# Kernel tuning notes

Hardware: AMD Instinct MI355X
Metric: run time of the kernel (lower is better)

## Reference

```python
import jax, jax.numpy as jnp
import numpy as np

B, S, DIM = 2, 2048, 1024
H, DH = 16, 64  # num_head, head_dim


def setup_inputs() -> dict:
    key = jax.random.key(0)
    ks = jax.random.split(key, 9)
    s = 1.0 / np.sqrt(DIM)
    s2 = 1.0 / np.sqrt(H * DH)
    return {
        "X": jax.random.normal(ks[0], (B, S, DIM), dtype=jnp.float32),
        "mask": jnp.ones((B, S), dtype=jnp.float32),
        "Wq": jax.random.normal(ks[1], (DIM, H * DH), dtype=jnp.float32) * s,
        "bq": jax.random.normal(ks[2], (H * DH,), dtype=jnp.float32) * s,
        "Wk": jax.random.normal(ks[3], (DIM, H * DH), dtype=jnp.float32) * s,
        "bk": jax.random.normal(ks[4], (H * DH,), dtype=jnp.float32) * s,
        "Wv": jax.random.normal(ks[5], (DIM, H * DH), dtype=jnp.float32) * s,
        "bv": jax.random.normal(ks[6], (H * DH,), dtype=jnp.float32) * s,
        "Wo": jax.random.normal(ks[7], (H * DH, DIM), dtype=jnp.float32) * s2,
        "bo": jax.random.normal(ks[8], (DIM,), dtype=jnp.float32) * s2,
    }


def _split_heads(x):
    # [B,S,H*DH] -> [B,H,S,DH]
    return x.reshape(B, S, H, DH).transpose(0, 2, 1, 3)


def reference(X, mask, Wq, bq, Wk, bk, Wv, bv, Wo, bo):
    Q = _split_heads(X @ Wq + bq)
    K = _split_heads(X @ Wk + bk)
    V = _split_heads(X @ Wv + bv)
    # scores: [B,H,S,S]
    dot = jnp.einsum("bhqd,bhkd->bhqk", Q, K) / np.sqrt(DH).astype(np.float32)
    dot = dot - 1000000.0 * (1.0 - mask[:, None, None, :])
    attn = jax.nn.softmax(dot, axis=-1)
    ctx = jnp.einsum("bhqk,bhkd->bhqd", attn, V)
    # combine heads: [B,S,H*DH]
    ctx = ctx.transpose(0, 2, 1, 3).reshape(B, S, H * DH)
    return ctx @ Wo + bo
```

## Files before the change

kernel.cpp:

```cpp
#include <hip/hip_runtime.h>
#include <hip/hip_bf16.h>
#include <math.h>

#define BB 2
#define SS 2048
#define DIM 1024
#define NH 16
#define DH 64

typedef __bf16 bf16x8 __attribute__((ext_vector_type(8)));
typedef float f32x4 __attribute__((ext_vector_type(4)));
typedef float f32x16 __attribute__((ext_vector_type(16)));
typedef unsigned int u32x4 __attribute__((ext_vector_type(4)));

#define PENL2 (1000000.0f * 1.44269504f)

#define VMW(N) asm volatile("s_waitcnt vmcnt(" #N ")" ::: "memory")

__device__ __forceinline__ void glds16(const __hip_bfloat16* g, __hip_bfloat16* l) {
    __builtin_amdgcn_global_load_lds(
        (const __attribute__((address_space(1))) void*)g,
        (__attribute__((address_space(3))) void*)l, 16, 0, 0);
}

__device__ __forceinline__ void glds4(const float* g, float* l) {
    __builtin_amdgcn_global_load_lds(
        (const __attribute__((address_space(1))) void*)g,
        (__attribute__((address_space(3))) void*)l, 4, 0, 0);
}

__device__ __forceinline__ unsigned short f2bf(float x) {
    unsigned int u = __builtin_bit_cast(unsigned int, x);
    return (unsigned short)((u + 0x8000u) >> 16);
}

__device__ __forceinline__ unsigned int pk2bf(float a, float b) {
#if __has_builtin(__builtin_amdgcn_cvt_pk_bf16_f32)
    typedef __bf16 bf16x2 __attribute__((ext_vector_type(2)));
    bf16x2 p = __builtin_amdgcn_cvt_pk_bf16_f32(a, b);
    return __builtin_bit_cast(unsigned int, p);
#else
    return (unsigned int)f2bf(a) | ((unsigned int)f2bf(b) << 16);
#endif
}

__device__ __forceinline__ float fexp2(float x) {
#if __has_builtin(__builtin_amdgcn_exp2f)
    return __builtin_amdgcn_exp2f(x);
#else
    return exp2f(x);
#endif
}

__device__ __forceinline__ float frcp(float x) {
#if __has_builtin(__builtin_amdgcn_rcpf)
    return __builtin_amdgcn_rcpf(x);
#else
    return 1.0f / x;
#endif
}

__global__ void prep(const float* __restrict__ X,
                     const float* __restrict__ Wq, const float* __restrict__ Wk,
                     const float* __restrict__ Wv, const float* __restrict__ Wo,
                     const float* __restrict__ mask, float* __restrict__ pf,
                     __hip_bfloat16* __restrict__ T4, ushort4* __restrict__ Xbf) {
    int z = blockIdx.z;
    int t = threadIdx.x;
    if (z == 4) {
        int c = blockIdx.y * 32 + blockIdx.x;
        const float4* in = (const float4*)X;
#pragma unroll
        for (int k = 0; k < 4; ++k) {
            int i = c * 1024 + k * 256 + t;
            float4 v = in[i];
            ushort4 h;
            h.x = f2bf(v.x); h.y = f2bf(v.y); h.z = f2bf(v.z); h.w = f2bf(v.w);
            Xbf[i] = h;
        }
        if (c < 16) {
            int i = c * 256 + t;
            pf[i] = -PENL2 * (1.0f - mask[i]);
        }
        return;
    }
    const float* W = (z == 0) ? Wq : (z == 1) ? Wk : (z == 2) ? Wv : Wo;
    __hip_bfloat16* Thi = T4 + (size_t)z * DIM * DIM;
    __shared__ float tile[32][33];
    int k0 = blockIdx.x * 32, n0 = blockIdx.y * 32;
    int r = t >> 3, c = (t & 7) << 2;
    float4 v = *(const float4*)&W[(size_t)(k0 + r) * DIM + n0 + c];
    tile[r][c] = v.x; tile[r][c + 1] = v.y; tile[r][c + 2] = v.z; tile[r][c + 3] = v.w;
    __syncthreads();
    size_t base = (size_t)(n0 + r) * DIM + k0 + c;
#pragma unroll
    for (int i = 0; i < 4; ++i)
        ((unsigned short*)Thi)[base + i] = f2bf(tile[c + i][r]);
}

#define BM 128
#define BK 32
#define QSCALE (0.125f * 1.44269504f)
template <int TBN>
__global__ __launch_bounds__(512, 6) void gemm_bf(
    const __hip_bfloat16* __restrict__ A, const __hip_bfloat16* __restrict__ B,
    const float* __restrict__ b0, const float* __restrict__ b1, const float* __restrict__ b2,
    __hip_bfloat16* __restrict__ oq, __hip_bfloat16* __restrict__ ok,
    __hip_bfloat16* __restrict__ ov, float* __restrict__ of32, int mode) {
    __shared__ alignas(16) __hip_bfloat16 sA[3][BM * BK];
    __shared__ alignas(16) __hip_bfloat16 sB[3][TBN * BK];
    const int K = 1024;
    const int JF = TBN / 64;
    int tid = threadIdx.x;
    int wave = tid >> 6, lane = tid & 63, quad = lane >> 4, l16 = lane & 15;

    int nbx = gridDim.x;
    int nwg = nbx * gridDim.y;
    int bid = blockIdx.y * nbx + blockIdx.x;
    int swz = (bid & 7) * (nwg >> 3) + (bid >> 3);
    int m0 = (swz / nbx) * BM, n0 = (swz % nbx) * TBN;
    int mo = (wave >> 2) * 64, no = (wave & 3) * (TBN / 4);

    f32x4 acc[4][JF];
#pragma unroll
    for (int i = 0; i < 4; ++i)
#pragma unroll
        for (int j = 0; j < JF; ++j) acc[i][j] = (f32x4){0.f, 0.f, 0.f, 0.f};

    int ar = tid >> 2;
    int c4 = tid & 3;
    int cs = c4 ^ ((ar >> 1) & 3);
    const __hip_bfloat16* gA = A + (size_t)(m0 + ar) * K + cs * 8;
    const __hip_bfloat16* gB = B + (size_t)(n0 + ar) * K + cs * 8;
    int ldst = ar * BK + c4 * 8;
    bool stgB = (ar < TBN);

    auto STG = [&](int bb, int k0) {
        glds16(gA + k0, &sA[bb][ldst]);
        if (stgB) glds16(gB + k0, &sB[bb][ldst]);
    };

    STG(0, 0);
    STG(1, BK);
    int cur = 0;
    for (int it = 0; it < 32; ++it) {
        int k0 = it * BK;
        if (it < 30) {
            int nb = cur + 2; if (nb >= 3) nb -= 3;
            STG(nb, k0 + 2 * BK);
            if (stgB) { VMW(4); } else { VMW(2); }
        } else if (it == 30) {
            if (stgB) { VMW(2); } else { VMW(1); }
        } else {
            VMW(0);
        }
        __builtin_amdgcn_s_barrier();

        bf16x8 a_h[4], b_h[JF];
#pragma unroll
        for (int i = 0; i < 4; ++i) {
            int rr = mo + i * 16 + l16;
            int ph = quad ^ ((rr >> 1) & 3);
            a_h[i] = *(const bf16x8*)&sA[cur][rr * BK + ph * 8];
        }
#pragma unroll
        for (int j = 0; j < JF; ++j) {
            int rr = no + j * 16 + l16;
            int ph = quad ^ ((rr >> 1) & 3);
            b_h[j] = *(const bf16x8*)&sB[cur][rr * BK + ph * 8];
        }
        __builtin_amdgcn_s_setprio(1);
#pragma unroll
        for (int i = 0; i < 4; ++i)
#pragma unroll
            for (int j = 0; j < JF; ++j)
                acc[i][j] = __builtin_amdgcn_mfma_f32_16x16x32_bf16(a_h[i], b_h[j], acc[i][j], 0, 0, 0);
        __builtin_amdgcn_s_setprio(0);
        __builtin_amdgcn_s_barrier();
        cur = (cur == 2) ? 0 : cur + 1;
    }

    int which = (mode == 1) ? (n0 >> 10) : 0;
    const float* bp = (mode == 0) ? b0 : (which == 0) ? b0 : (which == 1) ? b1 : b2;
#pragma unroll
    for (int i = 0; i < 4; ++i)
#pragma unroll
        for (int j = 0; j < JF; ++j) {
            int gmb = m0 + mo + i * 16 + quad * 4;
            int gn  = n0 + no + j * 16 + l16;
            int nn  = gn & 1023;
            float bb = bp[(mode == 0) ? gn : nn];
#pragma unroll
            for (int r = 0; r < 4; ++r) {
                int gm = gmb + r;
                float v = acc[i][j][r] + bb;
                if (mode == 0) {
                    of32[(size_t)gm * 1024 + gn] = v;
                } else {
                    int b = gm >> 11, s = gm & 2047, h = nn >> 6, d = nn & 63;
                    if (which == 0)
                        ((unsigned short*)oq)[(((size_t)(b * NH + h)) * SS + s) * DH + d] = f2bf(v * QSCALE);
                    else if (which == 1)
                        ((unsigned short*)ok)[(((size_t)(b * NH + h)) * SS + s) * DH + d] = f2bf(v);
                    else
                        ((unsigned short*)ov)[(((size_t)(b * NH + h)) * DH + d) * SS + s] = f2bf(v);
                }
            }
        }
}

__global__ __launch_bounds__(512, 4) void gemm_of(
    const __hip_bfloat16* __restrict__ O1, const __hip_bfloat16* __restrict__ O2,
    const float* __restrict__ l1, const float* __restrict__ l2,
    const __hip_bfloat16* __restrict__ Bw,
    const float* __restrict__ bias, float* __restrict__ out) {
    __shared__ alignas(16) __hip_bfloat16 sA[2][BM * BK];
    __shared__ alignas(16) __hip_bfloat16 sB[2][64 * BK];
    int tid = threadIdx.x;
    int wave = tid >> 6, lane = tid & 63, quad = lane >> 4, l16 = lane & 15;

    int nbx = gridDim.x;
    int nwg = nbx * gridDim.y;
    int bid = blockIdx.y * nbx + blockIdx.x;
    int swz = (bid & 7) * (nwg >> 3) + (bid >> 3);
    int m0 = (swz / nbx) * BM, n0 = (swz % nbx) * 64;
    int mo = (wave >> 2) * 64, no = (wave & 3) * 16;

    f32x4 acc[4];
#pragma unroll
    for (int i = 0; i < 4; ++i) acc[i] = (f32x4){0.f, 0.f, 0.f, 0.f};

    int ar = tid >> 2;
    int c4 = tid & 3;
    int cs = c4 ^ ((ar >> 1) & 3);
    int m  = m0 + ar;
    int bq16 = (m >> 11) * NH;
    int sq   = m & 2047;
    const __hip_bfloat16* gO1 = O1 + (size_t)m * 1024 + cs * 8;
    const __hip_bfloat16* gO2 = O2 + (size_t)m * 1024 + cs * 8;
    const __hip_bfloat16* gB  = Bw + (size_t)(n0 + ar) * 1024 + cs * 8;
    int ldst = ar * BK + c4 * 8;
    bool stgB = (ar < 64);

    bf16x8 n1 = *(const bf16x8*)(gO1);
    bf16x8 n2 = *(const bf16x8*)(gO2);
    float  nl = l1[(size_t)bq16 * SS + sq] + l2[(size_t)bq16 * SS + sq];
    if (stgB) glds16(gB, &sB[0][ldst]);
    {
        float linv = frcp(nl);
        unsigned int p0 = pk2bf(((float)n1[0] + (float)n2[0]) * linv,
                                ((float)n1[1] + (float)n2[1]) * linv);
        unsigned int p1 = pk2bf(((float)n1[2] + (float)n2[2]) * linv,
                                ((float)n1[3] + (float)n2[3]) * linv);
        unsigned int p2 = pk2bf(((float)n1[4] + (float)n2[4]) * linv,
                                ((float)n1[5] + (float)n2[5]) * linv);
        unsigned int p3 = pk2bf(((float)n1[6] + (float)n2[6]) * linv,
                                ((float)n1[7] + (float)n2[7]) * linv);
        u32x4 pw; pw.x = p0; pw.y = p1; pw.z = p2; pw.w = p3;
        *(bf16x8*)&sA[0][ldst] = __builtin_bit_cast(bf16x8, pw);
    }
    __syncthreads();

    int cur = 0;
    for (int it = 0; it < 32; ++it) {
        if (it < 31) {
            int k0n = (it + 1) * BK;
            n1 = *(const bf16x8*)(gO1 + k0n);
            n2 = *(const bf16x8*)(gO2 + k0n);
            size_t bhq = (size_t)(bq16 + (k0n >> 6)) * SS + sq;
            nl = l1[bhq] + l2[bhq];
            if (stgB) glds16(gB + k0n, &sB[cur ^ 1][ldst]);
        }

        bf16x8 a_h[4], b_h;
#pragma unroll
        for (int i = 0; i < 4; ++i) {
            int rr = mo + i * 16 + l16;
            int ph = quad ^ ((rr >> 1) & 3);
            a_h[i] = *(const bf16x8*)&sA[cur][rr * BK + ph * 8];
        }
        {
            int rr = no + l16;
            int ph = quad ^ ((rr >> 1) & 3);
            b_h = *(const bf16x8*)&sB[cur][rr * BK + ph * 8];
        }
        __builtin_amdgcn_s_setprio(1);
#pragma unroll
        for (int i = 0; i < 4; ++i)
            acc[i] = __builtin_amdgcn_mfma_f32_16x16x32_bf16(a_h[i], b_h, acc[i], 0, 0, 0);
        __builtin_amdgcn_s_setprio(0);

        if (it < 31) {
            float linv = frcp(nl);
            unsigned int p0 = pk2bf(((float)n1[0] + (float)n2[0]) * linv,
                                    ((float)n1[1] + (float)n2[1]) * linv);
            unsigned int p1 = pk2bf(((float)n1[2] + (float)n2[2]) * linv,
                                    ((float)n1[3] + (float)n2[3]) * linv);
            unsigned int p2 = pk2bf(((float)n1[4] + (float)n2[4]) * linv,
                                    ((float)n1[5] + (float)n2[5]) * linv);
            unsigned int p3 = pk2bf(((float)n1[6] + (float)n2[6]) * linv,
                                    ((float)n1[7] + (float)n2[7]) * linv);
            u32x4 pw; pw.x = p0; pw.y = p1; pw.z = p2; pw.w = p3;
            *(bf16x8*)&sA[cur ^ 1][ldst] = __builtin_bit_cast(bf16x8, pw);
        }
        __syncthreads();
        cur ^= 1;
    }

#pragma unroll
    for (int i = 0; i < 4; ++i) {
        int gmb = m0 + mo + i * 16 + quad * 4;
        int gn  = n0 + no + l16;
        float bb = bias[gn];
#pragma unroll
        for (int r = 0; r < 4; ++r)
            out[(size_t)(gmb + r) * 1024 + gn] = acc[i][r] + bb;
    }
}

__global__ __launch_bounds__(256, 4) void flash_split(
        const __hip_bfloat16* __restrict__ Q,
        const __hip_bfloat16* __restrict__ K,
        const __hip_bfloat16* __restrict__ Vt,
        const float* __restrict__ pf,
        __hip_bfloat16* __restrict__ Op0, __hip_bfloat16* __restrict__ Op1,
        float* __restrict__ lp0, float* __restrict__ lp1) {
    int bidl = blockIdx.x + (blockIdx.y << 4) + (blockIdx.z << 9);
    int w = (bidl & 7) * 128 + (bidl >> 3);
    int q0 = (w & 15) * 128;
    int bh = (w >> 4) & 31;
    int z  = w >> 9;
    int b = bh >> 4, h = bh & (NH - 1);
    __hip_bfloat16* Op = z ? Op1 : Op0;
    float*          lp = z ? lp1 : lp0;
    int tid = threadIdx.x;
    int wave = tid >> 6, lane = tid & 63;
    int l31 = lane & 31, hi = lane >> 5, l7 = lane & 7;

    __shared__ alignas(16) __hip_bfloat16 sK[2][64 * 64];
    __shared__ alignas(16) __hip_bfloat16 sV[2][64 * 64];
    __shared__ alignas(16) float sPF[2][64];

    const __hip_bfloat16* Qrow = Q + ((size_t)bh * SS + q0 + wave * 32 + l31) * DH;
    bf16x8 aq[4];
#pragma unroll
    for (int d_ = 0; d_ < 4; ++d_)
        aq[d_] = *(const bf16x8*)(Qrow + d_ * 16 + 8 * hi);

    const __hip_bfloat16* Kb = K + (size_t)bh * SS * DH;
    const __hip_bfloat16* Vb = Vt + (size_t)bh * DH * SS;
    const float* pfp = pf + b * SS;

    f32x16 z16;
#pragma unroll
    for (int r = 0; r < 16; ++r) z16[r] = 0.f;
    f32x16 O[2];
    O[0] = z16; O[1] = z16;
    f32x4 ls = (f32x4){0.f, 0.f, 0.f, 0.f};

    int xo[4];
#pragma unroll
    for (int c = 0; c < 4; ++c) xo[c] = ((((c << 1) | hi) ^ l7) << 4);

    int r8 = lane >> 3, c8 = lane & 7;
    int ck = c8 ^ r8;

    const int kbeg = z * (SS / 2);
    const int NT = (SS / 2) / 64;

    auto STAGE = [&](int bb, int k0) {
#pragma unroll
        for (int cc = 0; cc < 2; ++cc) {
            int row = cc * 32 + wave * 8 + r8;
            glds16(Kb + (size_t)(k0 + row) * DH + ck * 8, &sK[bb][row * 64 + c8 * 8]);
            glds16(Vb + (size_t)row * SS + k0 + ck * 8,  &sV[bb][row * 64 + c8 * 8]);
        }
        if (wave == 0)
            glds4(pfp + k0 + lane, &sPF[bb][0]);
    };

    STAGE(0, kbeg);
    __syncthreads();
    int cur = 0;
    for (int t = 0; t < NT; ++t) {
        int k0 = kbeg + t * 64;
        if (t + 1 < NT) STAGE(cur ^ 1, k0 + 64);
#pragma unroll
        for (int tt = 0; tt < 2; ++tt) {
            const char* pK = (const char*)&sK[cur][(tt * 32 + l31) * 64];
            bf16x8 kf[4];
#pragma unroll
            for (int d_ = 0; d_ < 4; ++d_)
                kf[d_] = *(const bf16x8*)(pK + xo[d_]);
            f32x16 st;
#pragma unroll
            for (int g = 0; g < 4; ++g) {
                f32x4 pv = *(const f32x4*)&sPF[cur][32 * tt + 8 * g + 4 * hi];
#pragma unroll
                for (int j = 0; j < 4; ++j) st[4 * g + j] = pv[j];
            }
            __builtin_amdgcn_s_setprio(1);
#pragma unroll
            for (int d_ = 0; d_ < 4; ++d_)
                st = __builtin_amdgcn_mfma_f32_32x32x16_bf16(kf[d_], aq[d_], st, 0, 0, 0);
            __builtin_amdgcn_s_setprio(0);

#pragma unroll
            for (int g = 0; g < 4; ++g) {
#pragma unroll
                for (int j = 0; j < 4; ++j)
                    st[4 * g + j] = fexp2(st[4 * g + j]);
                ls[0] += st[4 * g];     ls[1] += st[4 * g + 1];
                ls[2] += st[4 * g + 2]; ls[3] += st[4 * g + 3];
            }

            unsigned int u[8];
#pragma unroll
            for (int g = 0; g < 4; ++g) {
                u[2 * g]     = pk2bf(st[4 * g],     st[4 * g + 1]);
                u[2 * g + 1] = pk2bf(st[4 * g + 2], st[4 * g + 3]);
            }

#pragma unroll
            for (int kk = 0; kk < 2; ++kk) {
                unsigned int w0 = u[4 * kk],     w2 = u[4 * kk + 2];
                unsigned int w1 = u[4 * kk + 1], w3 = u[4 * kk + 3];
                asm("v_permlane32_swap_b32 %0, %1" : "+v"(w0), "+v"(w2));
                asm("v_permlane32_swap_b32 %0, %1" : "+v"(w1), "+v"(w3));
                u32x4 paw; paw.x = w0; paw.y = w1; paw.z = w2; paw.w = w3;
                bf16x8 pa = __builtin_bit_cast(bf16x8, paw);
                int ks = 2 * tt + kk;
                __builtin_amdgcn_s_setprio(1);
#pragma unroll
                for (int dt_ = 0; dt_ < 2; ++dt_) {
                    const char* pV = (const char*)&sV[cur][(dt_ * 32 + l31) * 64];
                    bf16x8 vf = *(const bf16x8*)(pV + xo[ks]);
                    O[dt_] = __builtin_amdgcn_mfma_f32_32x32x16_bf16(pa, vf, O[dt_], 0, 0, 0);
                }
                __builtin_amdgcn_s_setprio(0);
            }
        }
        __syncthreads();
        cur ^= 1;
    }

    unsigned short* op = (unsigned short*)Op;
    int qb = q0 + wave * 32;
#pragma unroll
    for (int dt_ = 0; dt_ < 2; ++dt_)
#pragma unroll
        for (int r = 0; r < 16; ++r) {
            int qq = (r & 3) + 8 * (r >> 2) + 4 * hi;
            op[((size_t)b * SS + qb + qq) * (NH * DH) + h * DH + dt_ * 32 + l31] =
                f2bf(O[dt_][r]);
        }
    float lt = ls[0] + ls[1] + ls[2] + ls[3];
    lt += __shfl_xor(lt, 32, 64);
    if (hi == 0)
        lp[(size_t)bh * SS + qb + l31] = lt;
}

extern "C" void kernel_launch(void* const* d_in, const int* in_sizes, int n_in,
                              void* d_out, int out_size, void* d_ws, size_t ws_size,
                              hipStream_t stream) {
    const float* X    = (const float*)d_in[0];
    const float* mask = (const float*)d_in[1];
    const float* Wq   = (const float*)d_in[2];
    const float* bq   = (const float*)d_in[3];
    const float* Wk   = (const float*)d_in[4];
    const float* bk   = (const float*)d_in[5];
    const float* Wv   = (const float*)d_in[6];
    const float* bv   = (const float*)d_in[7];
    const float* Wo   = (const float*)d_in[8];
    const float* bo   = (const float*)d_in[9];
    float* out = (float*)d_out;

    const size_t MB = 1u << 20;
    char* ws = (char*)d_ws;
    __hip_bfloat16* Xbf = (__hip_bfloat16*)(ws);
    __hip_bfloat16* Op0 = (__hip_bfloat16*)(ws + 8 * MB);
    __hip_bfloat16* Wt4 = (__hip_bfloat16*)(ws + 16 * MB);
    float*          lp0 = (float*)(ws + 24 * MB);
    float*          lp1 = (float*)(ws + 25 * MB);
    float*          pf  = (float*)(ws + 26 * MB);
    __hip_bfloat16* Qw  = (__hip_bfloat16*)(ws + 32 * MB);
    __hip_bfloat16* Kw  = (__hip_bfloat16*)(ws + 40 * MB);
    __hip_bfloat16* Vt  = (__hip_bfloat16*)(ws + 48 * MB);
    __hip_bfloat16* Op1 = (__hip_bfloat16*)(ws + 56 * MB);
    __hip_bfloat16* Wot = Wt4 + (size_t)3 * DIM * DIM;

    dim3 pgrd(32, 32, 5);
    prep<<<pgrd, 256, 0, stream>>>(X, Wq, Wk, Wv, Wo, mask, pf, Wt4, (ushort4*)Xbf);

    dim3 qkvgrd(3 * DIM / 128, (BB * SS) / BM);
    gemm_bf<128><<<qkvgrd, 512, 0, stream>>>(Xbf, Wt4, bq, bk, bv,
                                             Qw, Kw, Vt, nullptr, 1);

    dim3 agrd(SS / 128, BB * NH, 2);
    flash_split<<<agrd, 256, 0, stream>>>(Qw, Kw, Vt, pf, Op0, Op1, lp0, lp1);

    dim3 ogrd(DIM / 64, (BB * SS) / BM);
    gemm_of<<<ogrd, 512, 0, stream>>>(Op0, Op1, lp0, lp1, Wot, bo, out);
}
```

Baseline: 211.6 us.

## Triple-buffer output-projection GEMM with two-stage-ahead prefetch and explicit waitcnts

Reworks the output-projection GEMM (which also merges the two flash-split partials) from a double-buffered to a triple-buffered LDS pipeline. Global loads of the O partials, the l sums and the weight tile are now issued two K-steps ahead, with explicit vmcnt/lgkmcnt waits and raw barriers in place of __syncthreads. The loop is unrolled by two so the register staging alternates between two sets. This is meant to hide global-load latency behind the MFMAs, at the cost of 1.5x LDS, more live registers (possible lower occupancy), and fragile hand-counted waitcnt values.

```diff
diff --git a/kernel.cpp b/kernel.cpp
--- a/kernel.cpp
+++ b/kernel.cpp
@@ -16,6 +16,7 @@
 #define PENL2 (1000000.0f * 1.44269504f)
 
 #define VMW(N) asm volatile("s_waitcnt vmcnt(" #N ")" ::: "memory")
+#define LGKM0() asm volatile("s_waitcnt lgkmcnt(0)" ::: "memory")
 
 __device__ __forceinline__ void glds16(const __hip_bfloat16* g, __hip_bfloat16* l) {
     __builtin_amdgcn_global_load_lds(
@@ -214,8 +215,8 @@
     const float* __restrict__ l1, const float* __restrict__ l2,
     const __hip_bfloat16* __restrict__ Bw,
     const float* __restrict__ bias, float* __restrict__ out) {
-    __shared__ alignas(16) __hip_bfloat16 sA[2][BM * BK];
-    __shared__ alignas(16) __hip_bfloat16 sB[2][64 * BK];
+    __shared__ alignas(16) __hip_bfloat16 sA[3][BM * BK];
+    __shared__ alignas(16) __hip_bfloat16 sB[3][64 * BK];
     int tid = threadIdx.x;
     int wave = tid >> 6, lane = tid & 63, quad = lane >> 4, l16 = lane & 15;
 
@@ -242,69 +243,75 @@
     int ldst = ar * BK + c4 * 8;
     bool stgB = (ar < 64);
 
-    bf16x8 n1 = *(const bf16x8*)(gO1);
-    bf16x8 n2 = *(const bf16x8*)(gO2);
-    float  nl = l1[(size_t)bq16 * SS + sq] + l2[(size_t)bq16 * SS + sq];
-    if (stgB) glds16(gB, &sB[0][ldst]);
-    {
-        float linv = frcp(nl);
-        unsigned int p0 = pk2bf(((float)n1[0] + (float)n2[0]) * linv,
-                                ((float)n1[1] + (float)n2[1]) * linv);
-        unsigned int p1 = pk2bf(((float)n1[2] + (float)n2[2]) * linv,
-                                ((float)n1[3] + (float)n2[3]) * linv);
-        unsigned int p2 = pk2bf(((float)n1[4] + (float)n2[4]) * linv,
-                                ((float)n1[5] + (float)n2[5]) * linv);
-        unsigned int p3 = pk2bf(((float)n1[6] + (float)n2[6]) * linv,
-                                ((float)n1[7] + (float)n2[7]) * linv);
-        u32x4 pw; pw.x = p0; pw.y = p1; pw.z = p2; pw.w = p3;
-        *(bf16x8*)&sA[0][ldst] = __builtin_bit_cast(bf16x8, pw);
-    }
+#define OF_XFORM(N1, N2, NL, BUF)                                              \
+    {                                                                          \
+        float linv = frcp(NL);                                                 \
+        unsigned int p0 = pk2bf(((float)N1[0]+(float)N2[0])*linv,              \
+                                ((float)N1[1]+(float)N2[1])*linv);             \
+        unsigned int p1 = pk2bf(((float)N1[2]+(float)N2[2])*linv,              \
+                                ((float)N1[3]+(float)N2[3])*linv);             \
+        unsigned int p2 = pk2bf(((float)N1[4]+(float)N2[4])*linv,              \
+                                ((float)N1[5]+(float)N2[5])*linv);             \
+        unsigned int p3 = pk2bf(((float)N1[6]+(float)N2[6])*linv,              \
+                                ((float)N1[7]+(float)N2[7])*linv);             \
+        u32x4 pw_; pw_.x = p0; pw_.y = p1; pw_.z = p2; pw_.w = p3;             \
+        *(bf16x8*)&sA[BUF][ldst] = __builtin_bit_cast(bf16x8, pw_);            \
+    }
+
+#define OF_LOAD(N1, N2, NL, KOFF)                                              \
+    {                                                                          \
+        N1 = *(const bf16x8*)(gO1 + (KOFF));                                   \
+        N2 = *(const bf16x8*)(gO2 + (KOFF));                                   \
+        size_t bhq_ = (size_t)(bq16 + ((KOFF) >> 6)) * SS + sq;                \
+        NL = l1[bhq_] + l2[bhq_];                                              \
+        if (stgB) glds16(gB + (KOFF), &sB[(KOFF / BK) % 3][ldst]);             \
+    }
+
+#define OF_STEP(IT, P1, P2, PL, L1_, L2_, LL)                                  \
+    {                                                                          \
+        int it = (IT);                                                         \
+        if (it < 30) { OF_LOAD(L1_, L2_, LL, (it + 2) * BK); }                 \
+        if (it < 31) {                                                         \
+            int nxt = cur + 1; if (nxt >= 3) nxt -= 3;                         \
+            OF_XFORM(P1, P2, PL, nxt);                                         \
+        }                                                                      \
+        if (it < 30)      { if (stgB) { VMW(6); } else { VMW(4); } }           \
+        else if (it == 30){ if (stgB) { VMW(1); } else { VMW(0); } }           \
+        else              { VMW(0); }                                          \
+        LGKM0();                                                               \
+        __builtin_amdgcn_s_barrier();                                          \
+        bf16x8 a_h[4], b_h;                                                    \
+        _Pragma("unroll")                                                      \
+        for (int i = 0; i < 4; ++i) {                                          \
+            int rr = mo + i * 16 + l16;                                        \
+            int ph = quad ^ ((rr >> 1) & 3);                                   \
+            a_h[i] = *(const bf16x8*)&sA[cur][rr * BK + ph * 8];               \
+        }                                                                      \
+        {                                                                      \
+            int rr = no + l16;                                                 \
+            int ph = quad ^ ((rr >> 1) & 3);                                   \
+            b_h = *(const bf16x8*)&sB[cur][rr * BK + ph * 8];                  \
+        }                                                                      \
+        __builtin_amdgcn_s_setprio(1);                                         \
+        _Pragma("unroll")                                                      \
+        for (int i = 0; i < 4; ++i)                                            \
+            acc[i] = __builtin_amdgcn_mfma_f32_16x16x32_bf16(a_h[i], b_h, acc[i], 0, 0, 0); \
+        __builtin_amdgcn_s_setprio(0);                                         \
+        __builtin_amdgcn_s_barrier();                                          \
+        cur = (cur == 2) ? 0 : cur + 1;                                        \
+    }
+
+    bf16x8 na1, na2, nb1, nb2;
+    float  nla, nlb;
+    OF_LOAD(na1, na2, nla, 0);
+    OF_LOAD(nb1, nb2, nlb, BK);
+    OF_XFORM(na1, na2, nla, 0);
     __syncthreads();
 
     int cur = 0;
-    for (int it = 0; it < 32; ++it) {
-        if (it < 31) {
-            int k0n = (it + 1) * BK;
-            n1 = *(const bf16x8*)(gO1 + k0n);
-            n2 = *(const bf16x8*)(gO2 + k0n);
-            size_t bhq = (size_t)(bq16 + (k0n >> 6)) * SS + sq;
-            nl = l1[bhq] + l2[bhq];
-            if (stgB) glds16(gB + k0n, &sB[cur ^ 1][ldst]);
-        }
-
-        bf16x8 a_h[4], b_h;
-#pragma unroll
-        for (int i = 0; i < 4; ++i) {
-            int rr = mo + i * 16 + l16;
-            int ph = quad ^ ((rr >> 1) & 3);
-            a_h[i] = *(const bf16x8*)&sA[cur][rr * BK + ph * 8];
-        }
-        {
-            int rr = no + l16;
-            int ph = quad ^ ((rr >> 1) & 3);
-            b_h = *(const bf16x8*)&sB[cur][rr * BK + ph * 8];
-        }
-        __builtin_amdgcn_s_setprio(1);
-#pragma unroll
-        for (int i = 0; i < 4; ++i)
-            acc[i] = __builtin_amdgcn_mfma_f32_16x16x32_bf16(a_h[i], b_h, acc[i], 0, 0, 0);
-        __builtin_amdgcn_s_setprio(0);
-
-        if (it < 31) {
-            float linv = frcp(nl);
-            unsigned int p0 = pk2bf(((float)n1[0] + (float)n2[0]) * linv,
-                                    ((float)n1[1] + (float)n2[1]) * linv);
-            unsigned int p1 = pk2bf(((float)n1[2] + (float)n2[2]) * linv,
-                                    ((float)n1[3] + (float)n2[3]) * linv);
-            unsigned int p2 = pk2bf(((float)n1[4] + (float)n2[4]) * linv,
-                                    ((float)n1[5] + (float)n2[5]) * linv);
-            unsigned int p3 = pk2bf(((float)n1[6] + (float)n2[6]) * linv,
-                                    ((float)n1[7] + (float)n2[7]) * linv);
-            u32x4 pw; pw.x = p0; pw.y = p1; pw.z = p2; pw.w = p3;
-            *(bf16x8*)&sA[cur ^ 1][ldst] = __builtin_bit_cast(bf16x8, pw);
-        }
-        __syncthreads();
-        cur ^= 1;
+    for (int it2 = 0; it2 < 32; it2 += 2) {
+        OF_STEP(it2,     nb1, nb2, nlb, na1, na2, nla);
+        OF_STEP(it2 + 1, na1, na2, nla, nb1, nb2, nlb);
     }
 
 #pragma unroll
@@ -316,6 +323,9 @@
         for (int r = 0; r < 4; ++r)
             out[(size_t)(gmb + r) * 1024 + gn] = acc[i][r] + bb;
     }
+#undef OF_STEP
+#undef OF_LOAD
+#undef OF_XFORM
 }
 
 __global__ __launch_bounds__(256, 4) void flash_split(
```

Measured after the change: 212.1 us. About the same (+0.2%).
